# Optimization experiments

Measured on AMD Instinct MI355X. Metric: run time of the kernel, lower is better.

## Reference

```python
import jax, jax.numpy as jnp
import numpy as np

EMBED_DIM = 1024
N_HEADS = 16
HEAD_DIM = EMBED_DIM // N_HEADS
EPS = 1e-6


def setup_inputs() -> dict:
    key = jax.random.key(0)
    k_x, k_wqkv, k_bqkv, k_wo, k_bo = jax.random.split(key, 5)
    B, T, C = 2, 2048, EMBED_DIM
    s = 1.0 / np.sqrt(C)
    return {
        "x": jax.random.normal(k_x, (B, T, C), dtype=jnp.float32),
        "w_qkv": jax.random.normal(k_wqkv, (C, 3 * C), dtype=jnp.float32) * s,
        "b_qkv": jax.random.normal(k_bqkv, (3 * C,), dtype=jnp.float32) * s,
        "w_out": jax.random.normal(k_wo, (C, C), dtype=jnp.float32) * s,
        "b_out": jax.random.normal(k_bo, (C,), dtype=jnp.float32) * s,
    }


def reference(x, w_qkv, b_qkv, w_out, b_out):
    B, T, C = x.shape
    H, D = N_HEADS, HEAD_DIM
    qkv = x @ w_qkv + b_qkv                       # [B,T,3C]
    q, k, v = jnp.split(qkv, 3, axis=-1)
    # [B,H,T,D]
    q = q.reshape(B, T, H, D).transpose(0, 2, 1, 3)
    k = k.reshape(B, T, H, D).transpose(0, 2, 1, 3)
    v = v.reshape(B, T, H, D).transpose(0, 2, 1, 3)
    dot = jnp.einsum("bhqd,bhkd->bhqk", q, k)     # [B,H,T,T]
    q_sq = jnp.sum(q * q, axis=-1)[..., :, None]  # [B,H,T,1]
    k_sq = jnp.sum(k * k, axis=-1)[..., None, :]  # [B,H,1,T]
    scores = (dot * dot) / (q_sq + k_sq - 2.0 * dot + EPS)
    causal = jnp.tril(jnp.ones((T, T), dtype=bool))
    scores = jnp.where(causal, scores, -jnp.inf)
    attn = jax.nn.softmax(scores, axis=-1)
    out = jnp.einsum("bhqk,bhkd->bhqd", attn, v)  # [B,H,T,D]
    out = out.transpose(0, 2, 1, 3).reshape(B, T, C)
    return out @ w_out + b_out
```

## Files before the change

### kernel.cpp

```cpp
#include <hip/hip_runtime.h>
#include <stdint.h>


#define TSEQ 2048
#define BATCH 2

typedef _Float16 f16x8 __attribute__((ext_vector_type(8)));
typedef float f32x4 __attribute__((ext_vector_type(4)));

#define MFMA16(a, b, c) __builtin_amdgcn_mfma_f32_16x16x32_f16(a, b, c, 0, 0, 0)

__device__ __forceinline__ unsigned short f2h(float f) {
  union { _Float16 h; unsigned short u; } v;
  v.h = (_Float16)f;
  return v.u;
}
__device__ __forceinline__ float h2f(unsigned short u) {
  union { unsigned short u; _Float16 h; } v;
  v.u = u;
  return (float)v.h;
}
__device__ __forceinline__ unsigned int pack2h(float lo, float hi) {
  return (unsigned int)f2h(lo) | ((unsigned int)f2h(hi) << 16);
}
__device__ __forceinline__ float sumsq_u32(unsigned int u) {
  float lo = h2f(u & 0xffffu);
  float hi = h2f(u >> 16);
  return lo * lo + hi * hi;
}
__device__ __forceinline__ void async_ld16(const void* g, const void* l) {
  __builtin_amdgcn_global_load_lds((const __attribute__((address_space(1))) void*)g,
                                   (__attribute__((address_space(3))) void*)l,
                                   16, 0, 0);
}
template <int CTRL>
__device__ __forceinline__ float dpp_max_step(float x) {
  float y = __uint_as_float((unsigned)__builtin_amdgcn_update_dpp(
      0, (int)__float_as_uint(x), CTRL, 0xf, 0xf, true));
  return fmaxf(x, y);
}
__device__ __forceinline__ float dpp_row_max(float x) {
  x = dpp_max_step<0x121>(x);
  x = dpp_max_step<0x122>(x);
  x = dpp_max_step<0x124>(x);
  x = dpp_max_step<0x128>(x);
  return x;
}

__global__ __launch_bounds__(256) void cvt_x(const float* __restrict__ src,
                                             unsigned short* __restrict__ dst) {
  const int i = (blockIdx.x * 256 + threadIdx.x) * 8;
  const float4 a = *(const float4*)(src + i);
  const float4 b = *(const float4*)(src + i + 4);
  uint4 o;
  o.x = pack2h(a.x, a.y); o.y = pack2h(a.z, a.w);
  o.z = pack2h(b.x, b.y); o.w = pack2h(b.z, b.w);
  *(uint4*)(dst + i) = o;
}

__global__ __launch_bounds__(256) void transpose_w(const float* __restrict__ src,
                                                   unsigned short* __restrict__ dst,
                                                   int K, int N) {
  __shared__ unsigned short tile[32][33];
  const int tx = threadIdx.x, ty = threadIdx.y;
  const int nb = blockIdx.x * 32, kb = blockIdx.y * 32;
#pragma unroll
  for (int i = 0; i < 4; i++)
    tile[ty + 8 * i][tx] = f2h(src[(size_t)(kb + ty + 8 * i) * N + nb + tx]);
  __syncthreads();
#pragma unroll
  for (int i = 0; i < 4; i++)
    dst[(size_t)(nb + ty + 8 * i) * K + kb + tx] = tile[tx][ty + 8 * i];
}

template <int TN, bool OUT_F32>
__global__ __launch_bounds__(256) void gemm_bt(const unsigned short* __restrict__ A,
                                               const unsigned short* __restrict__ Bt,
                                               const float* __restrict__ bias,
                                               void* __restrict__ Cp,
                                               int N, int K) {
  __shared__ __attribute__((aligned(16))) unsigned short Atile[128 * 32];
  __shared__ __attribute__((aligned(16))) unsigned short Btile[TN * 32];
  constexpr int NJ = TN / 32;
  const int tid = threadIdx.x;
  const int w = tid >> 6, lane = tid & 63;
  const int quad = lane >> 4, l15 = lane & 15;
  const int m0 = blockIdx.y * 128, n0 = blockIdx.x * TN;
  const int wr = w >> 1, wc = w & 1;
  const int nwc = wc * (TN / 2);
  f32x4 acc[4][NJ] = {};
  for (int kt = 0; kt < K; kt += 32) {
    __syncthreads();
#pragma unroll
    for (int it = 0; it < 2; it++) {
      const int c = it * 256 + tid;
      async_ld16(A + (size_t)(m0 + (c >> 2)) * K + kt + (c & 3) * 8,
                 &Atile[(size_t)(it * 256 + w * 64) * 8]);
    }
#pragma unroll
    for (int it = 0; it < TN / 64; it++) {
      const int c = it * 256 + tid;
      async_ld16(Bt + (size_t)(n0 + (c >> 2)) * K + kt + (c & 3) * 8,
                 &Btile[(size_t)(it * 256 + w * 64) * 8]);
    }
    __syncthreads();
    f16x8 af[4], bfr[NJ];
#pragma unroll
    for (int i = 0; i < 4; i++)
      af[i] = *(const f16x8*)&Atile[(wr * 64 + i * 16 + l15) * 32 + quad * 8];
#pragma unroll
    for (int j = 0; j < NJ; j++)
      bfr[j] = *(const f16x8*)&Btile[(nwc + j * 16 + l15) * 32 + quad * 8];
#pragma unroll
    for (int i = 0; i < 4; i++)
#pragma unroll
      for (int j = 0; j < NJ; j++)
        acc[i][j] = MFMA16(af[i], bfr[j], acc[i][j]);
  }
#pragma unroll
  for (int j = 0; j < NJ; j++) {
    const int n = n0 + nwc + j * 16 + l15;
    const float bv = bias[n];
#pragma unroll
    for (int i = 0; i < 4; i++) {
      const int mb = m0 + wr * 64 + i * 16 + quad * 4;
#pragma unroll
      for (int r = 0; r < 4; r++) {
        if constexpr (OUT_F32)
          ((float*)Cp)[(size_t)(mb + r) * N + n] = acc[i][j][r] + bv;
        else
          ((unsigned short*)Cp)[(size_t)(mb + r) * N + n] = f2h(acc[i][j][r] + bv);
      }
    }
  }
}

__global__ __launch_bounds__(256, 4) void yat_attn(const unsigned short* __restrict__ qkv,
                                                   unsigned short* __restrict__ outp) {
  __shared__ __attribute__((aligned(16))) unsigned short Qp[64 * 72];
  __shared__ __attribute__((aligned(16))) unsigned short Kp[64 * 72];
  __shared__ __attribute__((aligned(16))) unsigned short Vt[64 * 72];
  __shared__ __attribute__((aligned(16))) unsigned short Pl[64 * 72];
  __shared__ float qsq[64], ksq[64], bcast[64];
  const int tid = threadIdx.x;
  const int w = tid >> 6, lane = tid & 63;
  const int quad = lane >> 4, l15 = lane & 15;
  const int bh = blockIdx.x, b = bh >> 4, h = bh & 15;
  const int y = blockIdx.y;
  const int qt = (y < 8) ? 31 - y : (y < 16) ? y - 8 : (y < 24) ? 39 - y : y - 16;
  const unsigned short* base = qkv + (size_t)b * TSEQ * 3072 + h * 64;
  const int t = tid >> 2, dc = (tid & 3) * 16;
  const int d0 = tid & 31, tg8 = tid >> 5;

  {
    const unsigned short* g = base + (size_t)(qt * 64 + t) * 3072 + dc;
    uint4 v0 = *(const uint4*)g;
    uint4 v1 = *(const uint4*)(g + 8);
    *(uint4*)&Qp[t * 72 + dc] = v0;
    *(uint4*)&Qp[t * 72 + dc + 8] = v1;
    float s = sumsq_u32(v0.x) + sumsq_u32(v0.y) + sumsq_u32(v0.z) + sumsq_u32(v0.w) +
              sumsq_u32(v1.x) + sumsq_u32(v1.y) + sumsq_u32(v1.z) + sumsq_u32(v1.w);
    s += __shfl_xor(s, 1);
    s += __shfl_xor(s, 2);
    if ((tid & 3) == 0) qsq[t] = s;
  }
  __syncthreads();
  const f16x8 aq0 = *(const f16x8*)&Qp[(w * 16 + l15) * 72 + quad * 8];
  const f16x8 aq1 = *(const f16x8*)&Qp[(w * 16 + l15) * 72 + 32 + quad * 8];
  const f16x8 onesf = {(_Float16)1.f, (_Float16)1.f, (_Float16)1.f, (_Float16)1.f,
                       (_Float16)1.f, (_Float16)1.f, (_Float16)1.f, (_Float16)1.f};

  f32x4 accO[4] = {};
  float m_r[4] = {0.f, 0.f, 0.f, 0.f};
  float l_acc = 0.f;

  uint4 kreg0, kreg1;
  unsigned int vreg[8];
  {
    const unsigned short* gk = base + 1024 + (size_t)t * 3072 + dc;
    kreg0 = *(const uint4*)gk;
    kreg1 = *(const uint4*)(gk + 8);
    const unsigned short* gv = base + 2048 + (size_t)(tg8 * 8) * 3072 + 2 * d0;
#pragma unroll
    for (int s = 0; s < 8; s++)
      vreg[s] = *(const unsigned int*)(gv + (size_t)s * 3072);
  }

  for (int kt = 0; kt <= qt; kt++) {
    __syncthreads();
    {
      *(uint4*)&Kp[t * 72 + dc] = kreg0;
      *(uint4*)&Kp[t * 72 + dc + 8] = kreg1;
      float s = sumsq_u32(kreg0.x) + sumsq_u32(kreg0.y) + sumsq_u32(kreg0.z) +
                sumsq_u32(kreg0.w) + sumsq_u32(kreg1.x) + sumsq_u32(kreg1.y) +
                sumsq_u32(kreg1.z) + sumsq_u32(kreg1.w);
      s += __shfl_xor(s, 1);
      s += __shfl_xor(s, 2);
      if ((tid & 3) == 0) ksq[t] = s;
      uint4 LO, HI;
      LO.x = (vreg[0] & 0xffffu) | (vreg[1] << 16);
      LO.y = (vreg[2] & 0xffffu) | (vreg[3] << 16);
      LO.z = (vreg[4] & 0xffffu) | (vreg[5] << 16);
      LO.w = (vreg[6] & 0xffffu) | (vreg[7] << 16);
      HI.x = (vreg[0] >> 16) | (vreg[1] & 0xffff0000u);
      HI.y = (vreg[2] >> 16) | (vreg[3] & 0xffff0000u);
      HI.z = (vreg[4] >> 16) | (vreg[5] & 0xffff0000u);
      HI.w = (vreg[6] >> 16) | (vreg[7] & 0xffff0000u);
      *(uint4*)&Vt[(2 * d0) * 72 + tg8 * 8] = LO;
      *(uint4*)&Vt[(2 * d0 + 1) * 72 + tg8 * 8] = HI;
    }
    if (kt < qt) {
      const unsigned short* gk = base + 1024 + (size_t)((kt + 1) * 64 + t) * 3072 + dc;
      kreg0 = *(const uint4*)gk;
      kreg1 = *(const uint4*)(gk + 8);
      const unsigned short* gv =
          base + 2048 + (size_t)((kt + 1) * 64 + tg8 * 8) * 3072 + 2 * d0;
#pragma unroll
      for (int s = 0; s < 8; s++)
        vreg[s] = *(const unsigned int*)(gv + (size_t)s * 3072);
    }
    __syncthreads();

    f32x4 accS[4] = {};
#pragma unroll
    for (int nt = 0; nt < 4; nt++) {
      const f16x8 bk0 = *(const f16x8*)&Kp[(nt * 16 + l15) * 72 + quad * 8];
      const f16x8 bk1 = *(const f16x8*)&Kp[(nt * 16 + l15) * 72 + 32 + quad * 8];
      accS[nt] = MFMA16(aq0, bk0, accS[nt]);
      accS[nt] = MFMA16(aq1, bk1, accS[nt]);
    }
    const bool diag = (kt == qt);
    float pval[4][4];
    float tmax[4] = {0.f, 0.f, 0.f, 0.f};
#pragma unroll
    for (int nt = 0; nt < 4; nt++) {
#pragma unroll
      for (int r = 0; r < 4; r++) {
        const int ql = w * 16 + quad * 4 + r;
        const int tl = nt * 16 + l15;
        const float d = accS[nt][r];
        const float den = qsq[ql] + ksq[tl] - 2.f * d + 1e-6f;
        float s = d * d * __builtin_amdgcn_rcpf(den);
        if (diag && tl > ql) s = -1e30f;
        pval[nt][r] = s;
        tmax[r] = fmaxf(tmax[r], s);
      }
    }
    float alpha[4];
#pragma unroll
    for (int r = 0; r < 4; r++) {
      const float mn = fmaxf(m_r[r], dpp_row_max(tmax[r]));
      alpha[r] = __expf(m_r[r] - mn);
      m_r[r] = mn;
    }
#pragma unroll
    for (int nt = 0; nt < 4; nt++)
#pragma unroll
      for (int r = 0; r < 4; r++)
        Pl[(w * 16 + quad * 4 + r) * 72 + nt * 16 + l15] =
            f2h(__expf(pval[nt][r] - m_r[r]));
    if (l15 == 0) {
#pragma unroll
      for (int r = 0; r < 4; r++) bcast[w * 16 + quad * 4 + r] = alpha[r];
    }
    __syncthreads();

    const float am = bcast[w * 16 + l15];
#pragma unroll
    for (int i = 0; i < 4; i++) {
      accO[i][0] *= am; accO[i][1] *= am; accO[i][2] *= am; accO[i][3] *= am;
    }
    const f16x8 bp0 = *(const f16x8*)&Pl[(w * 16 + l15) * 72 + quad * 8];
    const f16x8 bp1 = *(const f16x8*)&Pl[(w * 16 + l15) * 72 + 32 + quad * 8];
    f32x4 accL = {};
    accL = MFMA16(onesf, bp0, accL);
    accL = MFMA16(onesf, bp1, accL);
#pragma unroll
    for (int i = 0; i < 4; i++) {
      const f16x8 av0 = *(const f16x8*)&Vt[(i * 16 + l15) * 72 + quad * 8];
      const f16x8 av1 = *(const f16x8*)&Vt[(i * 16 + l15) * 72 + 32 + quad * 8];
      accO[i] = MFMA16(av0, bp0, accO[i]);
      accO[i] = MFMA16(av1, bp1, accO[i]);
    }
    l_acc = l_acc * am + accL[0];
  }

  __syncthreads();
  const float linv = 1.0f / l_acc;
#pragma unroll
  for (int i = 0; i < 4; i++)
#pragma unroll
    for (int r = 0; r < 4; r++)
      Qp[(w * 16 + l15) * 72 + i * 16 + quad * 4 + r] = f2h(accO[i][r] * linv);
  __syncthreads();
  {
    uint4 o0 = *(const uint4*)&Qp[t * 72 + dc];
    uint4 o1 = *(const uint4*)&Qp[t * 72 + dc + 8];
    unsigned short* g = outp + (size_t)(b * TSEQ + qt * 64 + t) * 1024 + h * 64 + dc;
    *(uint4*)g = o0;
    *(uint4*)(g + 8) = o1;
  }
}

extern "C" void kernel_launch(void* const* d_in, const int* in_sizes, int n_in,
                              void* d_out, int out_size, void* d_ws, size_t ws_size,
                              hipStream_t stream) {
  (void)in_sizes; (void)n_in; (void)out_size; (void)ws_size;
  const float* x     = (const float*)d_in[0];
  const float* w_qkv = (const float*)d_in[1];
  const float* b_qkv = (const float*)d_in[2];
  const float* w_out = (const float*)d_in[3];
  const float* b_out = (const float*)d_in[4];
  float* out = (float*)d_out;

  unsigned short* wqkvT  = (unsigned short*)d_ws;
  unsigned short* woT    = wqkvT + (size_t)3072 * 1024;
  unsigned short* qkvws  = woT + (size_t)1024 * 1024;
  unsigned short* xh     = qkvws + (size_t)4096 * 3072;
  unsigned short* attnws = xh;

  cvt_x<<<dim3(4096 * 1024 / (256 * 8)), 256, 0, stream>>>(x, xh);
  transpose_w<<<dim3(3072 / 32, 1024 / 32), dim3(32, 8), 0, stream>>>(w_qkv, wqkvT, 1024, 3072);
  transpose_w<<<dim3(1024 / 32, 1024 / 32), dim3(32, 8), 0, stream>>>(w_out, woT, 1024, 1024);
  gemm_bt<128, false><<<dim3(3072 / 128, 4096 / 128), 256, 0, stream>>>(xh, wqkvT, b_qkv, qkvws, 3072, 1024);
  yat_attn<<<dim3(BATCH * 16, 32), 256, 0, stream>>>(qkvws, attnws);
  gemm_bt<64, true><<<dim3(1024 / 64, 4096 / 128), 256, 0, stream>>>(attnws, woT, b_out, out, 1024, 1024);
}
```

Before: 205.7 us.

## Keep attention probabilities in registers via transposed S and permlane swaps

Computes S transposed (K as the A operand) so each lane holds one query row. The row max then becomes a two-step cross-lane shuffle instead of DPP row reductions. The P tile is no longer written to and re-read from LDS: it is packed to f16 and rearranged into the MFMA B-operand layout with permlane32/permlane16 swaps. This removes the per-iteration Pl/bcast shared-memory traffic and one __syncthreads. It relies on gfx950 permlane swap builtins and on the swap mapping being correct.

```diff
diff --git a/kernel.cpp b/kernel.cpp
--- a/kernel.cpp
+++ b/kernel.cpp
@@ -6,7 +6,9 @@
 #define BATCH 2
 
 typedef _Float16 f16x8 __attribute__((ext_vector_type(8)));
+typedef __fp16 fp16x2 __attribute__((ext_vector_type(2)));
 typedef float f32x4 __attribute__((ext_vector_type(4)));
+typedef unsigned int u32x2 __attribute__((ext_vector_type(2)));
 
 #define MFMA16(a, b, c) __builtin_amdgcn_mfma_f32_16x16x32_f16(a, b, c, 0, 0, 0)
 
@@ -33,18 +35,10 @@
                                    (__attribute__((address_space(3))) void*)l,
                                    16, 0, 0);
 }
-template <int CTRL>
-__device__ __forceinline__ float dpp_max_step(float x) {
-  float y = __uint_as_float((unsigned)__builtin_amdgcn_update_dpp(
-      0, (int)__float_as_uint(x), CTRL, 0xf, 0xf, true));
-  return fmaxf(x, y);
-}
-__device__ __forceinline__ float dpp_row_max(float x) {
-  x = dpp_max_step<0x121>(x);
-  x = dpp_max_step<0x122>(x);
-  x = dpp_max_step<0x124>(x);
-  x = dpp_max_step<0x128>(x);
-  return x;
+__device__ __forceinline__ unsigned int pk_f16(float lo, float hi) {
+  union { fp16x2 h; unsigned int u; } c;
+  c.h = __builtin_amdgcn_cvt_pkrtz(lo, hi);
+  return c.u;
 }
 
 __global__ __launch_bounds__(256) void cvt_x(const float* __restrict__ src,
@@ -140,8 +134,7 @@
   __shared__ __attribute__((aligned(16))) unsigned short Qp[64 * 72];
   __shared__ __attribute__((aligned(16))) unsigned short Kp[64 * 72];
   __shared__ __attribute__((aligned(16))) unsigned short Vt[64 * 72];
-  __shared__ __attribute__((aligned(16))) unsigned short Pl[64 * 72];
-  __shared__ float qsq[64], ksq[64], bcast[64];
+  __shared__ float qsq[64], ksq[64];
   const int tid = threadIdx.x;
   const int w = tid >> 6, lane = tid & 63;
   const int quad = lane >> 4, l15 = lane & 15;
@@ -169,9 +162,11 @@
   const f16x8 aq1 = *(const f16x8*)&Qp[(w * 16 + l15) * 72 + 32 + quad * 8];
   const f16x8 onesf = {(_Float16)1.f, (_Float16)1.f, (_Float16)1.f, (_Float16)1.f,
                        (_Float16)1.f, (_Float16)1.f, (_Float16)1.f, (_Float16)1.f};
+  const int ql = w * 16 + l15;
+  const float qsq_eps = qsq[ql] + 1e-6f;
 
   f32x4 accO[4] = {};
-  float m_r[4] = {0.f, 0.f, 0.f, 0.f};
+  float m_run = 0.f;
   float l_acc = 0.f;
 
   uint4 kreg0, kreg1;
@@ -226,63 +221,73 @@
     for (int nt = 0; nt < 4; nt++) {
       const f16x8 bk0 = *(const f16x8*)&Kp[(nt * 16 + l15) * 72 + quad * 8];
       const f16x8 bk1 = *(const f16x8*)&Kp[(nt * 16 + l15) * 72 + 32 + quad * 8];
-      accS[nt] = MFMA16(aq0, bk0, accS[nt]);
-      accS[nt] = MFMA16(aq1, bk1, accS[nt]);
-    }
-    const bool diag = (kt == qt);
-    float pval[4][4];
-    float tmax[4] = {0.f, 0.f, 0.f, 0.f};
+      accS[nt] = MFMA16(bk0, aq0, accS[nt]);
+      accS[nt] = MFMA16(bk1, aq1, accS[nt]);
+    }
+    float pv[4][4];
 #pragma unroll
     for (int nt = 0; nt < 4; nt++) {
+      const f32x4 k4 = *(const f32x4*)&ksq[nt * 16 + quad * 4];
 #pragma unroll
       for (int r = 0; r < 4; r++) {
-        const int ql = w * 16 + quad * 4 + r;
-        const int tl = nt * 16 + l15;
         const float d = accS[nt][r];
-        const float den = qsq[ql] + ksq[tl] - 2.f * d + 1e-6f;
-        float s = d * d * __builtin_amdgcn_rcpf(den);
-        if (diag && tl > ql) s = -1e30f;
-        pval[nt][r] = s;
-        tmax[r] = fmaxf(tmax[r], s);
+        const float den = __builtin_fmaf(-2.f, d, k4[r] + qsq_eps);
+        pv[nt][r] = d * d * __builtin_amdgcn_rcpf(den);
       }
     }
-    float alpha[4];
-#pragma unroll
-    for (int r = 0; r < 4; r++) {
-      const float mn = fmaxf(m_r[r], dpp_row_max(tmax[r]));
-      alpha[r] = __expf(m_r[r] - mn);
-      m_r[r] = mn;
-    }
-#pragma unroll
-    for (int nt = 0; nt < 4; nt++)
-#pragma unroll
-      for (int r = 0; r < 4; r++)
-        Pl[(w * 16 + quad * 4 + r) * 72 + nt * 16 + l15] =
-            f2h(__expf(pval[nt][r] - m_r[r]));
-    if (l15 == 0) {
-#pragma unroll
-      for (int r = 0; r < 4; r++) bcast[w * 16 + quad * 4 + r] = alpha[r];
-    }
-    __syncthreads();
-
-    const float am = bcast[w * 16 + l15];
+    if (kt == qt) {
+#pragma unroll
+      for (int nt = 0; nt < 4; nt++)
+#pragma unroll
+        for (int r = 0; r < 4; r++)
+          if (nt * 16 + quad * 4 + r > ql) pv[nt][r] = -1e30f;
+    }
+    float tm = fmaxf(fmaxf(fmaxf(pv[0][0], pv[0][1]), fmaxf(pv[0][2], pv[0][3])),
+                     fmaxf(fmaxf(pv[1][0], pv[1][1]), fmaxf(pv[1][2], pv[1][3])));
+    tm = fmaxf(tm, fmaxf(fmaxf(fmaxf(pv[2][0], pv[2][1]), fmaxf(pv[2][2], pv[2][3])),
+                         fmaxf(fmaxf(pv[3][0], pv[3][1]), fmaxf(pv[3][2], pv[3][3]))));
+    tm = fmaxf(tm, __shfl_xor(tm, 16));
+    tm = fmaxf(tm, __shfl_xor(tm, 32));
+    const float mn = fmaxf(m_run, tm);
+    const float alpha = __expf(m_run - mn);
+    m_run = mn;
+    unsigned int pa[4], pb[4];
+#pragma unroll
+    for (int nt = 0; nt < 4; nt++) {
+      pa[nt] = pk_f16(__expf(pv[nt][0] - mn), __expf(pv[nt][1] - mn));
+      pb[nt] = pk_f16(__expf(pv[nt][2] - mn), __expf(pv[nt][3] - mn));
+    }
+    union { f16x8 v; unsigned int u[4]; } bp0, bp1;
+    {
+      u32x2 s0 = __builtin_amdgcn_permlane32_swap(pa[0], pa[1], false, false);
+      u32x2 s1 = __builtin_amdgcn_permlane16_swap(s0.x, s0.y, false, false);
+      bp0.u[0] = s1.x; bp0.u[2] = s1.y;
+      s0 = __builtin_amdgcn_permlane32_swap(pb[0], pb[1], false, false);
+      s1 = __builtin_amdgcn_permlane16_swap(s0.x, s0.y, false, false);
+      bp0.u[1] = s1.x; bp0.u[3] = s1.y;
+      s0 = __builtin_amdgcn_permlane32_swap(pa[2], pa[3], false, false);
+      s1 = __builtin_amdgcn_permlane16_swap(s0.x, s0.y, false, false);
+      bp1.u[0] = s1.x; bp1.u[2] = s1.y;
+      s0 = __builtin_amdgcn_permlane32_swap(pb[2], pb[3], false, false);
+      s1 = __builtin_amdgcn_permlane16_swap(s0.x, s0.y, false, false);
+      bp1.u[1] = s1.x; bp1.u[3] = s1.y;
+    }
 #pragma unroll
     for (int i = 0; i < 4; i++) {
-      accO[i][0] *= am; accO[i][1] *= am; accO[i][2] *= am; accO[i][3] *= am;
-    }
-    const f16x8 bp0 = *(const f16x8*)&Pl[(w * 16 + l15) * 72 + quad * 8];
-    const f16x8 bp1 = *(const f16x8*)&Pl[(w * 16 + l15) * 72 + 32 + quad * 8];
+      accO[i][0] *= alpha; accO[i][1] *= alpha;
+      accO[i][2] *= alpha; accO[i][3] *= alpha;
+    }
     f32x4 accL = {};
-    accL = MFMA16(onesf, bp0, accL);
-    accL = MFMA16(onesf, bp1, accL);
+    accL = MFMA16(onesf, bp0.v, accL);
+    accL = MFMA16(onesf, bp1.v, accL);
 #pragma unroll
     for (int i = 0; i < 4; i++) {
       const f16x8 av0 = *(const f16x8*)&Vt[(i * 16 + l15) * 72 + quad * 8];
       const f16x8 av1 = *(const f16x8*)&Vt[(i * 16 + l15) * 72 + 32 + quad * 8];
-      accO[i] = MFMA16(av0, bp0, accO[i]);
-      accO[i] = MFMA16(av1, bp1, accO[i]);
-    }
-    l_acc = l_acc * am + accL[0];
+      accO[i] = MFMA16(av0, bp0.v, accO[i]);
+      accO[i] = MFMA16(av1, bp1.v, accO[i]);
+    }
+    l_acc = l_acc * alpha + accL[0];
   }
 
   __syncthreads();
```

After: 195.8 us. -4.8%, faster.
